# Kernel optimization log

Measured on AMD Instinct MI355X. Metric: run time of the kernel, lower is better.

## Reference

```python
import jax, jax.numpy as jnp
import numpy as np

B, S, T = 4, 4096, 512
D_MODEL, D_TEXT = 1024, 768
H, KVH, HD = 16, 2, 64  # heads, kv heads, head_dim; rep = H // KVH
REP = H // KVH
EPS = 1e-5


def setup_inputs() -> dict:
    key = jax.random.key(0)
    k = jax.random.split(key, 6)
    std = 0.02
    return {
        "x": jax.random.normal(k[0], (B, S, D_MODEL), jnp.float32),
        "text_input": jax.random.normal(k[1], (B, T, D_TEXT), jnp.float32),
        "ln_w": jnp.ones((D_TEXT,), jnp.float32),
        "ln_b": jnp.zeros((D_TEXT,), jnp.float32),
        # weights stored as [in, out] (transposed torch Linear layout)
        "Wq": jax.random.normal(k[2], (D_MODEL, D_MODEL), jnp.float32) * std,
        "Wkv": jax.random.normal(k[3], (D_TEXT, 2 * KVH * HD), jnp.float32) * std,
        "Wout": jax.random.normal(k[4], (D_MODEL, D_MODEL), jnp.float32) * std,
        "bout": jnp.zeros((D_MODEL,), jnp.float32),
    }


def reference(x, text_input, ln_w, ln_b, Wq, Wkv, Wout, bout):
    # LayerNorm over d_text
    mu = jnp.mean(text_input, axis=-1, keepdims=True)
    var = jnp.var(text_input, axis=-1, keepdims=True)
    tn = (text_input - mu) * jax.lax.rsqrt(var + EPS) * ln_w + ln_b

    # Projections
    Q = (x @ Wq).reshape(B, S, KVH, REP, HD)          # heads are kv-major: h = g*REP + r
    KV = tn @ Wkv                                      # [B, T, 2*KVH*HD]
    K, V = jnp.split(KV, 2, axis=-1)
    K = K.reshape(B, T, KVH, HD)
    V = V.reshape(B, T, KVH, HD)

    # Grouped-query attention without materializing repeated K/V
    scale = 1.0 / np.sqrt(HD)
    scores = jnp.einsum('bsgrd,btgd->bgrst', Q, K) * scale  # [B,KVH,REP,S,T]
    attn = jax.nn.softmax(scores, axis=-1)
    O = jnp.einsum('bgrst,btgd->bsgrd', attn, V).reshape(B, S, D_MODEL)

    return O @ Wout + bout
```

## Files before the change

### kernel.cpp

```cpp
#include <hip/hip_runtime.h>
#include <hip/hip_bf16.h>


#define B_    4
#define S_    4096
#define T_    512
#define DM_   1024
#define DT_   768
#define H_    16
#define KVH_  2
#define HD_   64

#define GLOBAL_AS __attribute__((address_space(1)))
#define LDS_AS    __attribute__((address_space(3)))

typedef __bf16 bf16x8 __attribute__((ext_vector_type(8)));
typedef float  f32x4  __attribute__((ext_vector_type(4)));

__global__ __launch_bounds__(256) void cast_f32_bf16(const float* __restrict__ in,
                                                     __hip_bfloat16* __restrict__ out) {
    int i = blockIdx.x * 256 + threadIdx.x;
    float4 v = ((const float4*)in)[i];
    union { ushort4 u; __hip_bfloat16 h[4]; } p;
    p.h[0] = __float2bfloat16(v.x);
    p.h[1] = __float2bfloat16(v.y);
    p.h[2] = __float2bfloat16(v.z);
    p.h[3] = __float2bfloat16(v.w);
    ((ushort4*)out)[i] = p.u;
}

__global__ __launch_bounds__(256) void transpose_cast(const float* __restrict__ in,
                                                      __hip_bfloat16* __restrict__ out,
                                                      int R, int C) {
    __shared__ float tile[32][33];
    int tx = threadIdx.x, ty = threadIdx.y;
    int r0 = blockIdx.y * 32, c0 = blockIdx.x * 32;
#pragma unroll
    for (int k = 0; k < 4; k++)
        tile[ty + 8 * k][tx] = in[(size_t)(r0 + ty + 8 * k) * C + c0 + tx];
    __syncthreads();
#pragma unroll
    for (int k = 0; k < 4; k++)
        out[(size_t)(c0 + ty + 8 * k) * R + r0 + tx] = __float2bfloat16(tile[tx][ty + 8 * k]);
}

__global__ __launch_bounds__(256) void ln_kv_kernel(const float* __restrict__ text,
                                                    const float* __restrict__ lnw,
                                                    const float* __restrict__ lnb,
                                                    const float* __restrict__ Wkv,
                                                    __hip_bfloat16* __restrict__ Kg,
                                                    __hip_bfloat16* __restrict__ Vt) {
    __shared__ float tn[8][DT_];
    __shared__ float red[2][256];
    int tid = threadIdx.x;
    int b  = blockIdx.x >> 6;
    int t0 = (blockIdx.x & 63) * 8;

    for (int j = 0; j < 8; j++) {
        const float* row = text + (size_t)(b * T_ + t0 + j) * DT_;
        float v0 = row[tid], v1 = row[tid + 256], v2 = row[tid + 512];
        red[0][tid] = v0 + v1 + v2;
        red[1][tid] = v0 * v0 + v1 * v1 + v2 * v2;
        __syncthreads();
        for (int ofs = 128; ofs > 0; ofs >>= 1) {
            if (tid < ofs) { red[0][tid] += red[0][tid + ofs]; red[1][tid] += red[1][tid + ofs]; }
            __syncthreads();
        }
        float mu  = red[0][0] * (1.0f / DT_);
        float var = red[1][0] * (1.0f / DT_) - mu * mu;
        float rs  = rsqrtf(var + 1e-5f);
        tn[j][tid]       = (v0 - mu) * rs * lnw[tid]       + lnb[tid];
        tn[j][tid + 256] = (v1 - mu) * rs * lnw[tid + 256] + lnb[tid + 256];
        tn[j][tid + 512] = (v2 - mu) * rs * lnw[tid + 512] + lnb[tid + 512];
        __syncthreads();
    }

    float acc[8] = {0, 0, 0, 0, 0, 0, 0, 0};
    for (int k = 0; k < DT_; k++) {
        float w = Wkv[(size_t)k * 256 + tid];
#pragma unroll
        for (int j = 0; j < 8; j++) acc[j] += tn[j][k] * w;
    }
    int c = tid;
    int isV = c >> 7;
    int cc = c & 127, g = cc >> 6, d = cc & 63;
#pragma unroll
    for (int j = 0; j < 8; j++) {
        int t = t0 + j;
        __hip_bfloat16 hv = __float2bfloat16(acc[j]);
        if (!isV) Kg[((size_t)(b * KVH_ + g) * T_ + t) * HD_ + d] = hv;
        else      Vt[((size_t)(b * KVH_ + g) * HD_ + d) * T_ + t] = hv;
    }
}

template <int EPI>
__global__ __launch_bounds__(512, 2) void gemm256(const __hip_bfloat16* __restrict__ A,
                                                  const __hip_bfloat16* __restrict__ Bt,
                                                  void* __restrict__ Cout,
                                                  const float* __restrict__ bias,
                                                  float scale, int M, int N, int K) {
    __shared__ __bf16 lds[65536];
    const int tid = threadIdx.x;
    const int w = tid >> 6, lane = tid & 63, q = lane >> 4, cL = lane & 15;
    const int wm = w >> 2, wn = w & 3;
    const size_t m0 = (size_t)blockIdx.y * 256, n0 = (size_t)blockIdx.x * 256;
    const __bf16* Ab = (const __bf16*)A + m0 * K;
    const __bf16* Bb = (const __bf16*)Bt + n0 * K;
    const int NT = K >> 6;

    int srcoff[2], dstoff[2];
#pragma unroll
    for (int it = 0; it < 2; ++it) {
        int id = tid + it * 512;
        int r = id >> 3, u = (id & 7) ^ (r & 7);
        srcoff[it] = r * K + u * 8;
        dstoff[it] = id * 8;
    }

    const int swz0 = ((0 + q) ^ (cL & 7)) * 8;
    const int swz1 = ((4 + q) ^ (cL & 7)) * 8;
    const int baseA = (wm * 128 + cL) * 64;
    const int baseB = (wn * 64 + cL) * 64;

    f32x4 acc[8][4] = {};

    auto STAGE = [&](int isB, int j, int tt) {
        const __bf16* g = (isB ? Bb : Ab) + (size_t)j * 128 * K + (size_t)tt * 64;
        const int sb = (tt & 1) * 32768 + isB * 16384 + j * 8192;
#pragma unroll
        for (int it = 0; it < 2; ++it)
            __builtin_amdgcn_global_load_lds(
                (const GLOBAL_AS void*)(g + srcoff[it]),
                (LDS_AS void*)(&lds[sb + dstoff[it]]), 16, 0, 0);
    };

    STAGE(0, 0, 0); STAGE(0, 1, 0); STAGE(1, 0, 0); STAGE(1, 1, 0);
    if (NT > 1) { STAGE(0, 0, 1); STAGE(0, 1, 1); }
    asm volatile("s_waitcnt vmcnt(4)" ::: "memory");
    __builtin_amdgcn_s_barrier();
    __builtin_amdgcn_sched_barrier(0);

    for (int t = 0; t < NT; ++t) {
        const int sb = (t & 1) * 32768;
        const __bf16* As = lds + sb;
        const __bf16* Bs = lds + sb + 16384;
        bf16x8 af[4][2];
#pragma unroll
        for (int ph = 0; ph < 4; ++ph) {
            const int mh = ph >> 1, nh = ph & 1;
            if (nh == 0) {
#pragma unroll
                for (int m = 0; m < 4; ++m) {
                    int ro = baseA + mh * 4096 + m * 1024;
                    af[m][0] = *(const bf16x8*)&As[ro + swz0];
                    af[m][1] = *(const bf16x8*)&As[ro + swz1];
                }
            }
            bf16x8 bq[2][2];
#pragma unroll
            for (int n = 0; n < 2; ++n) {
                int ro = baseB + nh * 2048 + n * 1024;
                bq[n][0] = *(const bf16x8*)&Bs[ro + swz0];
                bq[n][1] = *(const bf16x8*)&Bs[ro + swz1];
            }
            if (ph == 0)      { if (t + 1 < NT) STAGE(1, 0, t + 1); }
            else if (ph == 1) { if (t + 1 < NT) STAGE(1, 1, t + 1); }
            else if (ph == 3 && t + 2 < NT) { STAGE(0, 0, t + 2); STAGE(0, 1, t + 2); }

            __builtin_amdgcn_s_barrier();
            __builtin_amdgcn_sched_barrier(0);
            __builtin_amdgcn_s_setprio(1);
#pragma unroll
            for (int m = 0; m < 4; ++m)
#pragma unroll
                for (int n = 0; n < 2; ++n) {
                    f32x4* a = &acc[mh * 4 + m][nh * 2 + n];
                    *a = __builtin_amdgcn_mfma_f32_16x16x32_bf16(af[m][0], bq[n][0], *a, 0, 0, 0);
                    *a = __builtin_amdgcn_mfma_f32_16x16x32_bf16(af[m][1], bq[n][1], *a, 0, 0, 0);
                }
            __builtin_amdgcn_s_setprio(0);
            if (ph == 3) {
                if (t + 2 < NT)      asm volatile("s_waitcnt vmcnt(4)" ::: "memory");
                else if (t + 1 < NT) asm volatile("s_waitcnt vmcnt(0)" ::: "memory");
            }
            __builtin_amdgcn_s_barrier();
            __builtin_amdgcn_sched_barrier(0);
        }
    }

#pragma unroll
    for (int jn = 0; jn < 4; ++jn) {
        size_t col = n0 + wn * 64 + jn * 16 + cL;
        float bb = 0.0f;
        if (EPI == 1) bb = bias[col];
#pragma unroll
        for (int im = 0; im < 8; ++im) {
            size_t r = m0 + wm * 128 + im * 16 + 4 * q;
#pragma unroll
            for (int ii = 0; ii < 4; ++ii) {
                float v = acc[im][jn][ii];
                if (EPI == 0)
                    ((__hip_bfloat16*)Cout)[(r + ii) * N + col] = __float2bfloat16(v * scale);
                else
                    ((float*)Cout)[(r + ii) * N + col] = v + bb;
            }
        }
    }
}

__global__ __launch_bounds__(256, 4) void attn_kernel(const __hip_bfloat16* __restrict__ Qs,
                                                      const __hip_bfloat16* __restrict__ Kg,
                                                      const __hip_bfloat16* __restrict__ Vt,
                                                      __hip_bfloat16* __restrict__ Oc) {
    __shared__ __bf16 Ks[64 * 64];
    __shared__ __bf16 Vs[64 * 64];
    __shared__ __bf16 Ps[4][1024];
    int tid = threadIdx.x;
    int w = tid >> 6, lane = tid & 63, q = lane >> 4, cL = lane & 15;
    int bh = blockIdx.y;
    int b = bh >> 4, h = bh & 15, g = h >> 3;
    int s0 = blockIdx.x * 128 + w * 32;

    const __bf16* Qb = (const __bf16*)Qs;
    const __bf16* Kb = (const __bf16*)Kg + (size_t)(b * KVH_ + g) * T_ * HD_;
    const __bf16* Vb = (const __bf16*)Vt + (size_t)(b * KVH_ + g) * HD_ * T_;
    __bf16* pw = &Ps[w][0];

    int ksoff[2], vsoff[2];
#pragma unroll
    for (int it = 0; it < 2; it++) {
        int U = tid + it * 256;
        int r = U >> 3, us = (U & 7) ^ (r & 7);
        ksoff[it] = r * HD_ + us * 8;
        vsoff[it] = r * T_  + us * 8;
    }

    bf16x8 aq[2][2];
#pragma unroll
    for (int mi = 0; mi < 2; mi++) {
        size_t base = ((size_t)(b * S_) + s0 + mi * 16 + cL) * DM_ + h * HD_ + 8 * q;
        aq[mi][0] = *(const bf16x8*)(Qb + base);
        aq[mi][1] = *(const bf16x8*)(Qb + base + 32);
    }

    float lpart[2][4] = {};
    f32x4 oacc[2][4] = {};

#pragma unroll 1
    for (int tc = 0; tc < 8; tc++) {
        int t0 = tc * 64;
#pragma unroll
        for (int it = 0; it < 2; it++) {
            int U = tid + it * 256;
            __builtin_amdgcn_global_load_lds(
                (const GLOBAL_AS void*)(Kb + (size_t)t0 * HD_ + ksoff[it]),
                (LDS_AS void*)(&Ks[U * 8]), 16, 0, 0);
            __builtin_amdgcn_global_load_lds(
                (const GLOBAL_AS void*)(Vb + t0 + vsoff[it]),
                (LDS_AS void*)(&Vs[U * 8]), 16, 0, 0);
        }
        __syncthreads();

        f32x4 sc[2][4];
#pragma unroll
        for (int nt = 0; nt < 4; nt++) {
            int R = 16 * nt + cL;
            bf16x8 k0 = *(const bf16x8*)&Ks[R * 64 + ((q ^ (R & 7)) * 8)];
            bf16x8 k1 = *(const bf16x8*)&Ks[R * 64 + (((4 + q) ^ (R & 7)) * 8)];
#pragma unroll
            for (int mi = 0; mi < 2; mi++) {
                f32x4 a = {0.f, 0.f, 0.f, 0.f};
                a = __builtin_amdgcn_mfma_f32_16x16x32_bf16(aq[mi][0], k0, a, 0, 0, 0);
                a = __builtin_amdgcn_mfma_f32_16x16x32_bf16(aq[mi][1], k1, a, 0, 0, 0);
                sc[mi][nt] = a;
            }
        }

#pragma unroll
        for (int mi = 0; mi < 2; mi++)
#pragma unroll
            for (int i = 0; i < 4; i++) {
                float ls = 0.f;
#pragma unroll
                for (int nt = 0; nt < 4; nt++) {
                    float e = __expf(sc[mi][nt][i]); sc[mi][nt][i] = e; ls += e;
                }
                lpart[mi][i] += ls;
            }

#pragma unroll
        for (int ksc = 0; ksc < 2; ksc++) {
#pragma unroll
            for (int mi = 0; mi < 2; mi++)
#pragma unroll
                for (int half = 0; half < 2; half++) {
                    int nt = 2 * ksc + half;
                    int tin = half * 16 + cL;
                    int off = mi * 512 + (((tin >> 3) * 16 + 4 * q) * 8) + (tin & 7);
#pragma unroll
                    for (int i = 0; i < 4; i++)
                        pw[off + i * 8] = (__bf16)sc[mi][nt][i];
                }
            bf16x8 pa0 = *(const bf16x8*)&pw[lane * 8];
            bf16x8 pa1 = *(const bf16x8*)&pw[512 + lane * 8];
#pragma unroll
            for (int nd = 0; nd < 4; nd++) {
                int D = 16 * nd + cL;
                bf16x8 bv = *(const bf16x8*)&Vs[D * 64 + (((4 * ksc + q) ^ (D & 7)) * 8)];
                oacc[0][nd] = __builtin_amdgcn_mfma_f32_16x16x32_bf16(pa0, bv, oacc[0][nd], 0, 0, 0);
                oacc[1][nd] = __builtin_amdgcn_mfma_f32_16x16x32_bf16(pa1, bv, oacc[1][nd], 0, 0, 0);
            }
        }
        __syncthreads();
    }

#pragma unroll
    for (int mi = 0; mi < 2; mi++) {
        float rinv[4];
#pragma unroll
        for (int i = 0; i < 4; i++) {
            float l = lpart[mi][i];
            l += __shfl_xor(l, 1); l += __shfl_xor(l, 2);
            l += __shfl_xor(l, 4); l += __shfl_xor(l, 8);
            rinv[i] = 1.0f / l;
        }
#pragma unroll
        for (int nd = 0; nd < 4; nd++)
#pragma unroll
            for (int i = 0; i < 4; i++) {
                float v = oacc[mi][nd][i] * rinv[i];
                size_t s = (size_t)(b * S_) + s0 + mi * 16 + 4 * q + i;
                Oc[s * DM_ + h * HD_ + nd * 16 + cL] = __float2bfloat16(v);
            }
    }
}

extern "C" void kernel_launch(void* const* d_in, const int* in_sizes, int n_in,
                              void* d_out, int out_size, void* d_ws, size_t ws_size,
                              hipStream_t stream) {
    const float* x    = (const float*)d_in[0];
    const float* text = (const float*)d_in[1];
    const float* lnw  = (const float*)d_in[2];
    const float* lnb  = (const float*)d_in[3];
    const float* Wq   = (const float*)d_in[4];
    const float* Wkv  = (const float*)d_in[5];
    const float* Wout = (const float*)d_in[6];
    const float* bout = (const float*)d_in[7];

    char* ws = (char*)d_ws;
    __hip_bfloat16* xbf = (__hip_bfloat16*)(ws);
    __hip_bfloat16* Qs  = (__hip_bfloat16*)(ws + 33554432);
    __hip_bfloat16* Wqt = (__hip_bfloat16*)(ws + 67108864);
    __hip_bfloat16* Wot = (__hip_bfloat16*)(ws + 69206016);
    __hip_bfloat16* Kg  = (__hip_bfloat16*)(ws + 71303168);
    __hip_bfloat16* Vtp = (__hip_bfloat16*)(ws + 71827456);

    cast_f32_bf16<<<dim3((B_ * S_ * DM_) / 4 / 256), dim3(256), 0, stream>>>(x, xbf);
    transpose_cast<<<dim3(32, 32), dim3(32, 8), 0, stream>>>(Wq, Wqt, DM_, DM_);
    transpose_cast<<<dim3(32, 32), dim3(32, 8), 0, stream>>>(Wout, Wot, DM_, DM_);
    ln_kv_kernel<<<dim3(B_ * T_ / 8), dim3(256), 0, stream>>>(text, lnw, lnb, Wkv, Kg, Vtp);

    gemm256<0><<<dim3(DM_ / 256, (B_ * S_) / 256), dim3(512), 0, stream>>>(
        xbf, Wqt, (void*)Qs, nullptr, 0.125f, B_ * S_, DM_, DM_);

    attn_kernel<<<dim3(S_ / 128, B_ * H_), dim3(256), 0, stream>>>(Qs, Kg, Vtp, xbf);

    gemm256<1><<<dim3(DM_ / 256, (B_ * S_) / 256), dim3(512), 0, stream>>>(
        xbf, Wot, d_out, bout, 1.0f, B_ * S_, DM_, DM_);
}
```

Before: 341.6 us.

## Split LayerNorm and KV projection into wave-reduced LN plus MFMA bf16 GEMM

Replaces the fused LayerNorm+KV-projection kernel, which did a scalar fp32 dot-product loop, with three kernels. A wave-shuffle LayerNorm writes bf16 normalized text. A transpose-cast prepares Wkv in bf16. A small MFMA tiled GEMM with double-buffered async global-to-LDS loads writes K and transposed V. This moves the KV projection onto matrix cores at the cost of two extra launches and bf16 rounding of the normalized input. The workspace region is reused from the Q buffer before Q is written.

```diff
diff --git a/kernel.cpp b/kernel.cpp
--- a/kernel.cpp
+++ b/kernel.cpp
@@ -44,52 +44,114 @@
         out[(size_t)(c0 + ty + 8 * k) * R + r0 + tx] = __float2bfloat16(tile[tx][ty + 8 * k]);
 }
 
-__global__ __launch_bounds__(256) void ln_kv_kernel(const float* __restrict__ text,
-                                                    const float* __restrict__ lnw,
-                                                    const float* __restrict__ lnb,
-                                                    const float* __restrict__ Wkv,
-                                                    __hip_bfloat16* __restrict__ Kg,
-                                                    __hip_bfloat16* __restrict__ Vt) {
-    __shared__ float tn[8][DT_];
-    __shared__ float red[2][256];
+__global__ __launch_bounds__(256) void ln_norm(const float* __restrict__ text,
+                                               const float* __restrict__ lnw,
+                                               const float* __restrict__ lnb,
+                                               __hip_bfloat16* __restrict__ tnb) {
     int tid = threadIdx.x;
-    int b  = blockIdx.x >> 6;
-    int t0 = (blockIdx.x & 63) * 8;
-
-    for (int j = 0; j < 8; j++) {
-        const float* row = text + (size_t)(b * T_ + t0 + j) * DT_;
-        float v0 = row[tid], v1 = row[tid + 256], v2 = row[tid + 512];
-        red[0][tid] = v0 + v1 + v2;
-        red[1][tid] = v0 * v0 + v1 * v1 + v2 * v2;
+    int w = tid >> 6, lane = tid & 63;
+    int row0 = blockIdx.x * 8 + w * 2;
+#pragma unroll
+    for (int rr = 0; rr < 2; ++rr) {
+        int row = row0 + rr;
+        const float4* src = (const float4*)(text + (size_t)row * DT_);
+        float4 v[3];
+        float s = 0.f, s2 = 0.f;
+#pragma unroll
+        for (int j = 0; j < 3; ++j) {
+            v[j] = src[lane + 64 * j];
+            s  += v[j].x + v[j].y + v[j].z + v[j].w;
+            s2 += v[j].x * v[j].x + v[j].y * v[j].y + v[j].z * v[j].z + v[j].w * v[j].w;
+        }
+#pragma unroll
+        for (int ofs = 1; ofs < 64; ofs <<= 1) {
+            s  += __shfl_xor(s, ofs);
+            s2 += __shfl_xor(s2, ofs);
+        }
+        float mu  = s * (1.0f / DT_);
+        float var = s2 * (1.0f / DT_) - mu * mu;
+        float rs  = rsqrtf(var + 1e-5f);
+#pragma unroll
+        for (int j = 0; j < 3; ++j) {
+            float4 wv = ((const float4*)lnw)[lane + 64 * j];
+            float4 bv = ((const float4*)lnb)[lane + 64 * j];
+            union { ushort4 u; __hip_bfloat16 h[4]; } p;
+            p.h[0] = __float2bfloat16((v[j].x - mu) * rs * wv.x + bv.x);
+            p.h[1] = __float2bfloat16((v[j].y - mu) * rs * wv.y + bv.y);
+            p.h[2] = __float2bfloat16((v[j].z - mu) * rs * wv.z + bv.z);
+            p.h[3] = __float2bfloat16((v[j].w - mu) * rs * wv.w + bv.w);
+            ((ushort4*)(tnb + (size_t)row * DT_))[lane + 64 * j] = p.u;
+        }
+    }
+}
+
+__global__ __launch_bounds__(256) void kv_gemm(const __hip_bfloat16* __restrict__ Atn,
+                                               const __hip_bfloat16* __restrict__ Wkvt,
+                                               __hip_bfloat16* __restrict__ Kg,
+                                               __hip_bfloat16* __restrict__ Vt) {
+    __shared__ __bf16 As[2][64 * 32];
+    __shared__ __bf16 Bs[2][64 * 32];
+    const int tid = threadIdx.x;
+    const int w = tid >> 6, lane = tid & 63, q = lane >> 4, cL = lane & 15;
+    const size_t m0 = (size_t)blockIdx.y * 64, n0 = (size_t)blockIdx.x * 64;
+    const int K = DT_;
+    const int NT = K / 32;
+
+    int srcoff, dstoff;
+    {
+        int id = tid;
+        int sr = id >> 3, U = (id & 7) ^ (sr & 7);
+        int row = 2 * sr + (U >> 2), ko = (U & 3) * 8;
+        srcoff = row * K + ko;
+        dstoff = id * 8;
+    }
+    const __bf16* Ab = (const __bf16*)Atn + m0 * K;
+    const __bf16* Bb = (const __bf16*)Wkvt + n0 * K;
+
+    auto frag_off = [&](int R) {
+        return (R >> 1) * 64 + ((((R & 1) * 4 + q) ^ ((R >> 1) & 7)) * 8);
+    };
+    const int offA = frag_off(w * 16 + cL);
+    int offB[4];
+#pragma unroll
+    for (int nf = 0; nf < 4; ++nf) offB[nf] = frag_off(nf * 16 + cL);
+
+    f32x4 acc[4] = {};
+
+    auto STAGE = [&](int buf, int t) {
+        int k0 = t * 32;
+        __builtin_amdgcn_global_load_lds((const GLOBAL_AS void*)(Ab + srcoff + k0),
+                                         (LDS_AS void*)(&As[buf][dstoff]), 16, 0, 0);
+        __builtin_amdgcn_global_load_lds((const GLOBAL_AS void*)(Bb + srcoff + k0),
+                                         (LDS_AS void*)(&Bs[buf][dstoff]), 16, 0, 0);
+    };
+
+    STAGE(0, 0);
+    __syncthreads();
+    for (int t = 0; t < NT; ++t) {
+        int cur = t & 1;
+        if (t + 1 < NT) STAGE(cur ^ 1, t + 1);
+        bf16x8 af = *(const bf16x8*)&As[cur][offA];
+#pragma unroll
+        for (int nf = 0; nf < 4; ++nf) {
+            bf16x8 bf = *(const bf16x8*)&Bs[cur][offB[nf]];
+            acc[nf] = __builtin_amdgcn_mfma_f32_16x16x32_bf16(af, bf, acc[nf], 0, 0, 0);
+        }
         __syncthreads();
-        for (int ofs = 128; ofs > 0; ofs >>= 1) {
-            if (tid < ofs) { red[0][tid] += red[0][tid + ofs]; red[1][tid] += red[1][tid + ofs]; }
-            __syncthreads();
-        }
-        float mu  = red[0][0] * (1.0f / DT_);
-        float var = red[1][0] * (1.0f / DT_) - mu * mu;
-        float rs  = rsqrtf(var + 1e-5f);
-        tn[j][tid]       = (v0 - mu) * rs * lnw[tid]       + lnb[tid];
-        tn[j][tid + 256] = (v1 - mu) * rs * lnw[tid + 256] + lnb[tid + 256];
-        tn[j][tid + 512] = (v2 - mu) * rs * lnw[tid + 512] + lnb[tid + 512];
-        __syncthreads();
-    }
-
-    float acc[8] = {0, 0, 0, 0, 0, 0, 0, 0};
-    for (int k = 0; k < DT_; k++) {
-        float w = Wkv[(size_t)k * 256 + tid];
-#pragma unroll
-        for (int j = 0; j < 8; j++) acc[j] += tn[j][k] * w;
-    }
-    int c = tid;
-    int isV = c >> 7;
-    int cc = c & 127, g = cc >> 6, d = cc & 63;
-#pragma unroll
-    for (int j = 0; j < 8; j++) {
-        int t = t0 + j;
-        __hip_bfloat16 hv = __float2bfloat16(acc[j]);
-        if (!isV) Kg[((size_t)(b * KVH_ + g) * T_ + t) * HD_ + d] = hv;
-        else      Vt[((size_t)(b * KVH_ + g) * HD_ + d) * T_ + t] = hv;
+    }
+
+#pragma unroll
+    for (int nf = 0; nf < 4; ++nf) {
+        int n = (int)n0 + nf * 16 + cL;
+        int isV = n >> 7, g = (n >> 6) & 1, d = n & 63;
+#pragma unroll
+        for (int ii = 0; ii < 4; ++ii) {
+            int m = (int)m0 + w * 16 + 4 * q + ii;
+            int b = m >> 9, tt = m & 511;
+            __hip_bfloat16 hv = __float2bfloat16(acc[nf][ii]);
+            if (!isV) Kg[((size_t)(b * KVH_ + g) * T_ + tt) * HD_ + d] = hv;
+            else      Vt[((size_t)(b * KVH_ + g) * HD_ + d) * T_ + tt] = hv;
+        }
     }
 }
 
@@ -354,11 +416,18 @@
     __hip_bfloat16* Wot = (__hip_bfloat16*)(ws + 69206016);
     __hip_bfloat16* Kg  = (__hip_bfloat16*)(ws + 71303168);
     __hip_bfloat16* Vtp = (__hip_bfloat16*)(ws + 71827456);
+    __hip_bfloat16* tnb  = (__hip_bfloat16*)(ws + 33554432);
+    __hip_bfloat16* Wkvt = (__hip_bfloat16*)(ws + 33554432 + 3145728);
 
     cast_f32_bf16<<<dim3((B_ * S_ * DM_) / 4 / 256), dim3(256), 0, stream>>>(x, xbf);
     transpose_cast<<<dim3(32, 32), dim3(32, 8), 0, stream>>>(Wq, Wqt, DM_, DM_);
     transpose_cast<<<dim3(32, 32), dim3(32, 8), 0, stream>>>(Wout, Wot, DM_, DM_);
-    ln_kv_kernel<<<dim3(B_ * T_ / 8), dim3(256), 0, stream>>>(text, lnw, lnb, Wkv, Kg, Vtp);
+    transpose_cast<<<dim3(8, 24), dim3(32, 8), 0, stream>>>(Wkv, Wkvt, DT_, 2 * KVH_ * HD_);
+
+    ln_norm<<<dim3(B_ * T_ / 8), dim3(256), 0, stream>>>(text, lnw, lnb, tnb);
+
+    kv_gemm<<<dim3(2 * KVH_ * HD_ / 64, B_ * T_ / 64), dim3(256), 0, stream>>>(
+        tnb, Wkvt, Kg, Vtp);
 
     gemm256<0><<<dim3(DM_ / 256, (B_ * S_) / 256), dim3(512), 0, stream>>>(
         xbf, Wqt, (void*)Qs, nullptr, 0.125f, B_ * S_, DM_, DM_);
```

Result: faster. 301.7 us (-11.7%).
